# Kernel optimization log

Measured on AMD Instinct MI355X. Metric: run time of the kernel, lower is better.

The kernel has to match this reference:

```python
import jax, jax.numpy as jnp
import numpy as np

E, C, L, B = 8, 128, 1024, 32
FB = L // 2 + 1        # 513 freq bins
HD = 2 * FB            # 1026 hidden dim


def setup_inputs() -> dict:
    key = jax.random.key(0)
    ks = jax.random.split(key, 8)
    return {
        "X_time": jax.random.normal(ks[0], (B, C, L), jnp.float32),
        "bound_params": jax.random.normal(ks[1], (E - 1,), jnp.float32),
        "W1r": jax.random.normal(ks[2], (E, HD, FB), jnp.float32) * 0.1,
        "W1i": jax.random.normal(ks[3], (E, HD, FB), jnp.float32) * 0.1,
        "b1r": jnp.zeros((E, HD), jnp.float32),
        "b1i": jnp.zeros((E, HD), jnp.float32),
        "W2r": jax.random.normal(ks[4], (E, FB, HD), jnp.float32) * 0.1,
        "W2i": jax.random.normal(ks[5], (E, FB, HD), jnp.float32) * 0.1,
        "b2r": jnp.zeros((E, FB), jnp.float32),
        "b2i": jnp.zeros((E, FB), jnp.float32),
        "gate_W": jax.random.normal(ks[6], (E, FB), jnp.float32) * 0.1,
        "gate_b": jnp.zeros((E,), jnp.float32),
    }


def reference(X_time, bound_params, W1r, W1i, b1r, b1i, W2r, W2i, b2r, b2i, gate_W, gate_b):
    Bx, Cx, Lx = X_time.shape
    fb = Lx // 2 + 1
    e = W1r.shape[0]

    Xf = jnp.fft.rfft(X_time, axis=-1)                     # [B,C,FB] complex

    # learnable frequency-band binary masks
    raw = jax.nn.sigmoid(bound_params)
    bounds = jnp.sort(jnp.concatenate([jnp.zeros(1, raw.dtype), raw, jnp.ones(1, raw.dtype)]))
    idx = (bounds * (fb - 1)).astype(jnp.int32)
    starts = idx[:e]
    ends = jnp.concatenate([idx[1:e], jnp.array([fb], jnp.int32)])
    pos = jnp.arange(fb)
    masks = ((pos[None, :] >= starts[:, None]) & (pos[None, :] < ends[:, None])).astype(X_time.dtype)  # [E,FB]

    # masked spectra per expert, split into real/imag: [E,B,C,FB]
    m = masks[:, None, None, :]
    xr = Xf.real * m
    xi = Xf.imag * m

    # expert layer 1: complex linear (W [E,HD,FB]) + complex ReLU
    hr = jnp.einsum('ehf,ebcf->ebch', W1r, xr) - jnp.einsum('ehf,ebcf->ebch', W1i, xi) + b1r[:, None, None, :]
    hi = jnp.einsum('ehf,ebcf->ebch', W1r, xi) + jnp.einsum('ehf,ebcf->ebch', W1i, xr) + b1i[:, None, None, :]
    hr = jax.nn.relu(hr)
    hi = jax.nn.relu(hi)

    # expert layer 2: complex linear (W [E,FB,HD]) -> [E,B,C,FB]
    yr = jnp.einsum('efh,ebch->ebcf', W2r, hr) - jnp.einsum('efh,ebch->ebcf', W2i, hi) + b2r[:, None, None, :]
    yi = jnp.einsum('efh,ebch->ebcf', W2r, hi) + jnp.einsum('efh,ebch->ebcf', W2i, hr) + b2i[:, None, None, :]

    # gate: mean |Xf| over channels -> linear -> softmax over experts
    mag = jnp.mean(jnp.abs(Xf), axis=1)                    # [B,FB]
    gate = jax.nn.softmax(mag @ gate_W.T + gate_b, axis=-1)  # [B,E]

    comb_r = jnp.einsum('ebcf,be->bcf', yr, gate)
    comb_i = jnp.einsum('ebcf,be->bcf', yi, gate)
    return jnp.fft.irfft(jax.lax.complex(comb_r, comb_i), n=Lx, axis=-1)
```

## Files before the change

### kernel.cpp

```cpp
#include <hip/hip_runtime.h>
#include <hip/hip_bf16.h>
#include <math.h>

typedef __hip_bfloat16 bf16;
typedef __attribute__((ext_vector_type(8))) short short8;
typedef __attribute__((ext_vector_type(4))) float f32x4;

#define FB 513
#define HD 1026
#define NN 1024
#define MR 4096
#define NE 8
#define BATCH 32

#define XINT_LD 1280
#define BIAS_LD 1056
#define FINV_LD 1088
#define HP_LD   2080
#define B1_ROWS 2176
#define KCAT    16640
#define MAG_LD  520
#define FF_ROWS 1280

__device__ __forceinline__ void gload16(const void* g, void* l) {
    __builtin_amdgcn_global_load_lds((const __attribute__((address_space(1))) void*)g,
                                     (__attribute__((address_space(3))) void*)l, 16, 0, 0);
}
__device__ __forceinline__ bf16 f2b(float v) { return __float2bfloat16(v); }
__device__ __forceinline__ unsigned short f2bu(float v) {
    bf16 b = __float2bfloat16(v);
    return *reinterpret_cast<unsigned short*>(&b);
}
__device__ __forceinline__ float bu2f(unsigned short u) {
    return __uint_as_float(((unsigned)u) << 16);
}
__device__ __forceinline__ unsigned pack2(float a, float b) {
    return (unsigned)f2bu(a) | ((unsigned)f2bu(b) << 16);
}

__device__ __forceinline__ void xcd_swizzle(int* px, int* py) {
    int gx = gridDim.x;
    int orig = blockIdx.x + gx * blockIdx.y;
    int q = (gx * gridDim.y) >> 3;
    int wg = (orig & 7) * q + (orig >> 3);
    *px = wg % gx;
    *py = wg / gx;
}

__device__ __forceinline__ void compute_bounds(const float* __restrict__ bp, int* idx) {
    float b[9];
    b[0] = 0.0f; b[8] = 1.0f;
    for (int i = 0; i < 7; i++) b[i + 1] = 1.0f / (1.0f + expf(-bp[i]));
    for (int i = 1; i < 9; i++) { float v = b[i]; int j = i - 1;
        while (j >= 0 && b[j] > v) { b[j + 1] = b[j]; j--; } b[j + 1] = v; }
    for (int i = 0; i < 9; i++) idx[i] = (int)(b[i] * (float)(FB - 1));
}

#define N_FF  ((long)FF_ROWS * NN)
#define N_FI  (1024L * FINV_LD)
#define N_B1P ((long)NE * B1_ROWS * (XINT_LD / 2))
#define N_XP  ((long)MR * NN / 2)
#define N_PREP (N_FF + N_FI + N_B1P + N_XP)

__global__ void prep_bulk(const float* __restrict__ W1r, const float* __restrict__ W1i,
                          const float* __restrict__ X, const float* __restrict__ bp,
                          int* __restrict__ se,
                          bf16* __restrict__ Ffwd, bf16* __restrict__ Finv,
                          bf16* __restrict__ B1, bf16* __restrict__ Xb) {
    __shared__ int sse[16];
    if (threadIdx.x == 0) {
        int idx[9];
        compute_bounds(bp, idx);
        for (int e = 0; e < NE; e++) {
            sse[2 * e] = idx[e];
            sse[2 * e + 1] = (e < NE - 1) ? idx[e + 1] : FB;
        }
        if (blockIdx.x == 0)
            for (int k = 0; k < 16; k++) se[k] = sse[k];
    }
    __syncthreads();

    long i = (long)blockIdx.x * 256 + threadIdx.x;
    const float TWO_PI = 6.283185307179586f;
    if (i < N_FF) {
        int n = (int)(i >> 10), t = (int)(i & (NN - 1));
        float v = 0.0f;
        if (n < 2 * FB) {
            int f = n >> 1, k = (f * t) & (NN - 1);
            float s, c; sincosf(TWO_PI * (float)k / (float)NN, &s, &c);
            v = (n & 1) ? -s : c;
        }
        Ffwd[i] = f2b(v);
        return;
    }
    i -= N_FF;
    if (i < N_FI) {
        int t = (int)(i / FINV_LD), k = (int)(i % FINV_LD);
        float v = 0.0f;
        if (k < 2 * FB) {
            int f = k >> 1, kk = (f * t) & (NN - 1);
            float s, c; sincosf(TWO_PI * (float)kk / (float)NN, &s, &c);
            float cf = (f == 0 || f == FB - 1) ? 1.0f : 2.0f;
            float sc = cf * (1.0f / (float)NN);
            v = (k & 1) ? -s * sc : c * sc;
        }
        Finv[i] = f2b(v);
        return;
    }
    i -= N_FI;
    if (i < N_B1P) {
        int f = (int)(i % (XINT_LD / 2));
        long t = i / (XINT_LD / 2);
        int n = (int)(t % B1_ROWS);
        int e = (int)(t / B1_ROWS);
        float ve = 0.0f, vo = 0.0f;
        if (n < 2 * HD && f < FB && f >= sse[2 * e] && f < sse[2 * e + 1]) {
            int hi_part = (n >= HD);
            int h = hi_part ? n - HD : n;
            long wi = ((long)e * HD + h) * FB + f;
            float wr = W1r[wi], wim = W1i[wi];
            ve = hi_part ? wim : wr;
            vo = hi_part ? wr : -wim;
        }
        *(unsigned*)(B1 + ((size_t)(e * B1_ROWS + n)) * XINT_LD + 2 * f) = pack2(ve, vo);
        return;
    }
    i -= N_B1P;
    if (i < N_XP) {
        float2 v = ((const float2*)X)[i];
        *(unsigned*)(Xb + 2 * i) = pack2(v.x, v.y);
    }
}

__global__ void pack_B2t(const float* __restrict__ W2r, const float* __restrict__ W2i,
                         bf16* __restrict__ B2t) {
    __shared__ float sR[64][65], sI[64][65];
    int e = blockIdx.z;
    int f0 = blockIdx.x * 64;
    int h0 = blockIdx.y * 64;
    int tid = threadIdx.x;
#pragma unroll
    for (int rep = 0; rep < 16; rep++) {
        int idx = tid + rep * 256;
        int fl = idx >> 6, hl = idx & 63;
        int f = f0 + fl, h = h0 + hl;
        bool ok = (f < FB) && (h < HD);
        size_t wi = ((size_t)e * FB + f) * HD + h;
        sR[fl][hl] = ok ? W2r[wi] : 0.0f;
        sI[fl][hl] = ok ? W2i[wi] : 0.0f;
    }
    __syncthreads();
#pragma unroll
    for (int rep = 0; rep < 4; rep++) {
        int idx = tid + rep * 256;
        int hl = idx >> 4, ch = idx & 15;
        int h = h0 + hl;
        int c0 = 2 * f0 + ch * 8;
        if (c0 >= FINV_LD) continue;
        short8 lo, hi;
#pragma unroll
        for (int j = 0; j < 4; j++) {
            int fl = ch * 4 + j;
            float wr = sR[fl][hl], wim = sI[fl][hl];
            lo[2 * j]     = (short)f2bu(wr);
            lo[2 * j + 1] = (short)f2bu(wim);
            hi[2 * j]     = (short)f2bu(-wim);
            hi[2 * j + 1] = (short)f2bu(wr);
        }
        if (h < HD) {
            *(short8*)(B2t + ((size_t)e * HP_LD + h) * FINV_LD + c0) = lo;
            *(short8*)(B2t + ((size_t)e * HP_LD + HD + h) * FINV_LD + c0) = hi;
        } else if (HD + h < HP_LD) {
            short8 z = {};
            *(short8*)(B2t + ((size_t)e * HP_LD + HD + h) * FINV_LD + c0) = z;
        }
    }
}

__global__ void mag_kernel(const bf16* __restrict__ Xint, float* __restrict__ magp) {
    int b = blockIdx.x, g = blockIdx.y, t = threadIdx.x;
    float acc[3] = {0.0f, 0.0f, 0.0f};
    const bf16* base = Xint + ((size_t)b * 128 + g * 16) * XINT_LD;
    for (int c = 0; c < 16; c++) {
        const bf16* row = base + (size_t)c * XINT_LD;
#pragma unroll
        for (int kk = 0; kk < 3; kk++) {
            int f = t + 256 * kk;
            if (f < FB) {
                float xr = __bfloat162float(row[2 * f]);
                float xi = __bfloat162float(row[2 * f + 1]);
                acc[kk] += sqrtf(xr * xr + xi * xi);
            }
        }
    }
#pragma unroll
    for (int kk = 0; kk < 3; kk++) {
        int f = t + 256 * kk;
        if (f < FB) magp[((size_t)b * 8 + g) * MAG_LD + f] = acc[kk];
    }
}

__global__ void gate_bias_kernel(const float* __restrict__ magp, const float* __restrict__ gW,
                                 const float* __restrict__ gb, const float* __restrict__ b2r,
                                 const float* __restrict__ b2i, float* __restrict__ gate,
                                 float* __restrict__ biasCs) {
    __shared__ float sred[256];
    __shared__ float sg[8];
    int b = blockIdx.x, tid = threadIdx.x;
    int e = tid & 7, j = tid >> 3;
    float acc = 0.0f;
    for (int f = j; f < FB; f += 32) {
        float m = 0.0f;
#pragma unroll
        for (int g = 0; g < 8; g++) m += magp[((size_t)b * 8 + g) * MAG_LD + f];
        acc += m * (1.0f / 128.0f) * gW[e * FB + f];
    }
    sred[tid] = acc;
    __syncthreads();
    if (tid < 64) {
        float a = sred[tid] + sred[tid + 64] + sred[tid + 128] + sred[tid + 192];
        a += __shfl_xor(a, 8); a += __shfl_xor(a, 16); a += __shfl_xor(a, 32);
        float logit = a + gb[e];
        float mx = logit;
        mx = fmaxf(mx, __shfl_xor(mx, 1)); mx = fmaxf(mx, __shfl_xor(mx, 2)); mx = fmaxf(mx, __shfl_xor(mx, 4));
        float ex = expf(logit - mx);
        float sum = ex;
        sum += __shfl_xor(sum, 1); sum += __shfl_xor(sum, 2); sum += __shfl_xor(sum, 4);
        if (tid < 8) { float g_ = ex / sum; sg[tid] = g_; gate[b * NE + tid] = g_; }
    }
    __syncthreads();
    for (int c = tid; c < BIAS_LD; c += 256) {
        float v = 0.0f;
        if (c < 2 * FB) {
            int f = c >> 1;
            const float* bb = (c & 1) ? b2i : b2r;
#pragma unroll
            for (int ee = 0; ee < NE; ee++) v += sg[ee] * bb[ee * FB + f];
            float cf = (f == 0 || f == FB - 1) ? 1.0f : 2.0f;
            v *= cf * (1.0f / (float)NN);
        }
        biasCs[b * BIAS_LD + c] = v;
    }
}

__global__ void biasT_kernel(const float* __restrict__ biasCs, const bf16* __restrict__ Ffwd,
                             float* __restrict__ biasT) {
    int t = blockIdx.x * 256 + threadIdx.x;
    int b = blockIdx.y;
    float s = 0.0f;
    for (int c = 0; c < 2 * FB; c++)
        s += biasCs[b * BIAS_LD + c] * __bfloat162float(Ffwd[(size_t)c * NN + t]);
    biasT[b * NN + t] = s;
}

__global__ void reduce_out4(const bf16* __restrict__ planes, const float* __restrict__ biasT,
                            float* __restrict__ out) {
    long idx = (long)blockIdx.x * 256 + threadIdx.x;
    if (idx >= (long)MR * NN / 8) return;
    size_t base = (size_t)idx * 8;
    long r = base >> 10;
    int t = (int)(base & (NN - 1));
    float s[8] = {};
#pragma unroll
    for (int z = 0; z < 4; z++) {
        short8 v = *(const short8*)(planes + (size_t)z * MR * NN + base);
#pragma unroll
        for (int j = 0; j < 8; j++) s[j] += bu2f((unsigned short)v[j]);
    }
    const float* bT = biasT + (r >> 7) * NN + t;
    float4 o0 = {s[0] + bT[0], s[1] + bT[1], s[2] + bT[2], s[3] + bT[3]};
    float4 o1 = {s[4] + bT[4], s[5] + bT[5], s[6] + bT[6], s[7] + bT[7]};
    *(float4*)(out + base) = o0;
    *(float4*)(out + base + 4) = o1;
}

template <int EPI>
__global__ void gemm_mfma(const bf16* __restrict__ A, int lda,
                          const bf16* __restrict__ B, int ldb, size_t zBstride,
                          void* __restrict__ Cv, int ldc, size_t zCoff,
                          int N, int K, int kPerZ,
                          const int* __restrict__ se2,
                          const float* __restrict__ biasR, const float* __restrict__ biasI,
                          int zBias, const float* __restrict__ gate8) {
    __shared__ bf16 As[128 * 32];
    __shared__ bf16 Bs[128 * 32];
    int tid = threadIdx.x;
    int zz = blockIdx.z;
    int bx, by;
    xcd_swizzle(&bx, &by);
    int row0 = by * 128, col0 = bx * 128;
    const bf16* Bz = B + (size_t)zz * zBstride;

    int kS, kE;
    if (EPI == 1) { int s = se2[2 * zz], e = se2[2 * zz + 1]; kS = (2 * s) & ~31; kE = (2 * e + 31) & ~31; }
    else          { kS = zz * kPerZ; kE = min(K, kS + kPerZ); }

    f32x4 acc[4][4] = {};

    int lane = tid & 63, wid = tid >> 6;
    int wrB = (wid >> 1) << 6, wcB = (wid & 1) << 6;
    int lr = lane & 15, lk = (lane >> 4) << 3;

    int r_a = tid >> 2, c_a = (tid & 3) << 3;
    int r_b = (tid + 256) >> 2, c_b = ((tid + 256) & 3) << 3;

    for (int kt = kS; kt < kE; kt += 32) {
        gload16(A + (size_t)(row0 + r_a) * lda + kt + c_a, &As[(size_t)tid * 8]);
        gload16(A + (size_t)(row0 + r_b) * lda + kt + c_b, &As[((size_t)tid + 256) * 8]);
        gload16(Bz + (size_t)(col0 + r_a) * ldb + kt + c_a, &Bs[(size_t)tid * 8]);
        gload16(Bz + (size_t)(col0 + r_b) * ldb + kt + c_b, &Bs[((size_t)tid + 256) * 8]);
        __syncthreads();
        short8 av[4], bv[4];
#pragma unroll
        for (int m = 0; m < 4; m++)
            av[m] = *(const short8*)&As[(wrB + m * 16 + lr) * 32 + lk];
#pragma unroll
        for (int n = 0; n < 4; n++)
            bv[n] = *(const short8*)&Bs[(wcB + n * 16 + lr) * 32 + lk];
#pragma unroll
        for (int m = 0; m < 4; m++)
#pragma unroll
            for (int n = 0; n < 4; n++)
                acc[m][n] = __builtin_amdgcn_mfma_f32_16x16x32_bf16(av[m], bv[n], acc[m][n], 0, 0, 0);
        __syncthreads();
    }

    int r0 = row0 + wrB + ((lane >> 4) << 2);
    int c0i = col0 + wcB + (lane & 15);
    float g = (EPI == 1) ? gate8[(row0 >> 7) * NE + zz] : 0.0f;

#pragma unroll
    for (int m = 0; m < 4; m++)
#pragma unroll
        for (int n = 0; n < 4; n++) {
            int c = c0i + n * 16;
            if (c >= N) continue;
#pragma unroll
            for (int j = 0; j < 4; j++) {
                int r = r0 + m * 16 + j;
                float v = acc[m][n][j];
                if (EPI == 1) {
                    v += (c < HD) ? biasR[zz * zBias + c] : biasI[zz * zBias + c - HD];
                    v = fmaxf(v, 0.0f) * g;
                    ((bf16*)Cv + (size_t)zz * zCoff)[(size_t)r * ldc + c] = f2b(v);
                } else {
                    ((float*)Cv + (size_t)zz * zCoff)[(size_t)r * ldc + c] = v;
                }
            }
        }
}

__device__ __forceinline__ void stage_half(const bf16* gbase, int ld, int kt,
                                           bf16* ldsBase, int tid) {
#pragma unroll
    for (int j = 0; j < 2; j++) {
        int r = j * 64 + (tid >> 3);
        int sc = ((tid & 7) ^ ((tid >> 3) & 7)) * 8;
        gload16(gbase + (size_t)r * ld + kt + sc, ldsBase + j * 4096 + tid * 8);
    }
}

#define MF(a, b, c) __builtin_amdgcn_mfma_f32_16x16x32_bf16(a, b, c, 0, 0, 0)
#define RD(off) (*(const short8*)(bc + (off)))
#define LOADA(dst, FM)                                                        \
    dst[0] = RD(aBase + (FM) * 1024 + cb0);                                   \
    dst[1] = RD(aBase + (FM) * 1024 + cb1);                                   \
    dst[2] = RD(aBase + (FM + 1) * 1024 + cb0);                               \
    dst[3] = RD(aBase + (FM + 1) * 1024 + cb1);
#define CLUST(FM, av)                                                         \
    __builtin_amdgcn_s_setprio(1);                                            \
    acc[FM][0] = MF(av[0], b0[0], acc[FM][0]);                                \
    acc[FM][0] = MF(av[1], b1[0], acc[FM][0]);                                \
    acc[FM][1] = MF(av[0], b0[1], acc[FM][1]);                                \
    acc[FM][1] = MF(av[1], b1[1], acc[FM][1]);                                \
    acc[FM][2] = MF(av[0], b0[2], acc[FM][2]);                                \
    acc[FM][2] = MF(av[1], b1[2], acc[FM][2]);                                \
    acc[FM][3] = MF(av[0], b0[3], acc[FM][3]);                                \
    acc[FM][3] = MF(av[1], b1[3], acc[FM][3]);                                \
    acc[FM + 1][0] = MF(av[2], b0[0], acc[FM + 1][0]);                        \
    acc[FM + 1][0] = MF(av[3], b1[0], acc[FM + 1][0]);                        \
    acc[FM + 1][1] = MF(av[2], b0[1], acc[FM + 1][1]);                        \
    acc[FM + 1][1] = MF(av[3], b1[1], acc[FM + 1][1]);                        \
    acc[FM + 1][2] = MF(av[2], b0[2], acc[FM + 1][2]);                        \
    acc[FM + 1][2] = MF(av[3], b1[2], acc[FM + 1][2]);                        \
    acc[FM + 1][3] = MF(av[2], b0[3], acc[FM + 1][3]);                        \
    acc[FM + 1][3] = MF(av[3], b1[3], acc[FM + 1][3]);                        \
    __builtin_amdgcn_s_setprio(0);
#define PBAR { __builtin_amdgcn_sched_barrier(0); __builtin_amdgcn_s_barrier(); }

template <int SWZ>
__global__ __launch_bounds__(512, 2) void gemm8p(
        const bf16* __restrict__ A, int lda, const bf16* __restrict__ B, int ldb,
        bf16* __restrict__ C, int ldc, size_t zCoff,
        int tilesPerZ, int totTiles, int gx) {
    __shared__ bf16 sm[65536];
    int tid = threadIdx.x;
    int id = blockIdx.x;
    int bx, by, z;
    if (SWZ == 1) {
        int by_z = (id & 7) * 8 + (id >> 5);
        bx = (id >> 3) & 3;
        z = by_z >> 4;
        by = by_z & 15;
    } else {
        bx = id % gx; by = id / gx; z = 0;
    }
    int row0 = by * 256, col0 = bx * 256;
    int t0 = z * tilesPerZ;
    int nt = min(tilesPerZ, totTiles - t0);
    int kS = t0 * 64;

    const bf16* Ab = A + (size_t)row0 * lda;
    const bf16* Bb = B + (size_t)col0 * ldb;

    stage_half(Ab, lda, kS, sm, tid);
    stage_half(Ab + (size_t)128 * lda, lda, kS, sm + 8192, tid);
    stage_half(Bb, ldb, kS, sm + 16384, tid);
    stage_half(Bb + (size_t)128 * ldb, ldb, kS, sm + 24576, tid);

    f32x4 acc[8][4] = {};

    int l = tid & 63, w = tid >> 6;
    int wm = w >> 2, wn = w & 3;
    int lr = l & 15, lk4 = l >> 4;
    int swz = lr & 7;
    int cb0 = ((lk4) ^ swz) * 8;
    int cb1 = ((4 + lk4) ^ swz) * 8;
    int aBase = wm * 8192 + lr * 64;
    int bBase = 16384 + (wn >> 1) * 8192 + (wn & 1) * 4096 + lr * 64;

    for (int t = 0; t < nt; ++t) {
        const int cur = t & 1;
        const bf16* bc = sm + cur * 32768;
        bf16* bufN = sm + (cur ^ 1) * 32768;
        int ktn = kS + (t + 1) * 64;
        bool more = (t + 1) < nt;
        if (more) {
            stage_half(Ab, lda, ktn, bufN, tid);
            stage_half(Ab + (size_t)128 * lda, lda, ktn, bufN + 8192, tid);
            asm volatile("s_waitcnt vmcnt(4)" ::: "memory");
        } else {
            asm volatile("s_waitcnt vmcnt(0)" ::: "memory");
        }
        __builtin_amdgcn_s_barrier();
        __builtin_amdgcn_sched_barrier(0);
        short8 b0[4], b1[4], a0[4], a1[4], a2[4], a3[4];
#pragma unroll
        for (int n = 0; n < 4; n++) {
            b0[n] = RD(bBase + n * 1024 + cb0);
            b1[n] = RD(bBase + n * 1024 + cb1);
        }
        LOADA(a0, 0)
        LOADA(a1, 2)
        __builtin_amdgcn_sched_barrier(0);
        CLUST(0, a0)
        if (more) {
            stage_half(Bb, ldb, ktn, bufN + 16384, tid);
            stage_half(Bb + (size_t)128 * ldb, ldb, ktn, bufN + 24576, tid);
        }
        LOADA(a2, 4)
        PBAR
        CLUST(2, a1)
        LOADA(a3, 6)
        PBAR
        CLUST(4, a2)
        PBAR
        CLUST(6, a3)
        PBAR
    }

    bf16* Cp = C + (size_t)z * zCoff;
    int rb = row0 + wm * 128 + lk4 * 4;
    int cbase = col0 + wn * 64 + lr;
#pragma unroll
    for (int fm = 0; fm < 8; fm++)
#pragma unroll
        for (int n = 0; n < 4; n++)
#pragma unroll
            for (int j = 0; j < 4; j++)
                Cp[(size_t)(rb + fm * 16 + j) * ldc + cbase + n * 16] = f2b(acc[fm][n][j]);
}

extern "C" void kernel_launch(void* const* d_in, const int* in_sizes, int n_in,
                              void* d_out, int out_size, void* d_ws, size_t ws_size,
                              hipStream_t stream) {
    const float* X   = (const float*)d_in[0];
    const float* bp  = (const float*)d_in[1];
    const float* W1r = (const float*)d_in[2];
    const float* W1i = (const float*)d_in[3];
    const float* b1r = (const float*)d_in[4];
    const float* b1i = (const float*)d_in[5];
    const float* W2r = (const float*)d_in[6];
    const float* W2i = (const float*)d_in[7];
    const float* b2r = (const float*)d_in[8];
    const float* b2i = (const float*)d_in[9];
    const float* gW  = (const float*)d_in[10];
    const float* gb  = (const float*)d_in[11];
    float* out = (float*)d_out;

    const size_t SZH = (size_t)MR * HP_LD * 2;

    char* p = (char*)d_ws;
    auto alloc = [&](size_t bytes) -> char* {
        char* r = p; p += (bytes + 255) & ~255ULL; return r;
    };
    int*   se     = (int*)alloc(64 * 4);
    float* magp   = (float*)alloc((size_t)BATCH * 8 * MAG_LD * 4);
    float* gate   = (float*)alloc((size_t)BATCH * NE * 4);
    float* biasCs = (float*)alloc((size_t)BATCH * BIAS_LD * 4);
    float* biasT  = (float*)alloc((size_t)BATCH * NN * 4);
    bf16*  Ffwd   = (bf16*)alloc((size_t)FF_ROWS * NN * 2);
    bf16*  Finv   = (bf16*)alloc((size_t)NN * FINV_LD * 2);
    bf16*  B1     = (bf16*)alloc((size_t)NE * B1_ROWS * XINT_LD * 2);
    bf16*  B2t    = (bf16*)alloc((size_t)KCAT * FINV_LD * 2);
    bf16*  Xint   = (bf16*)alloc((size_t)MR * XINT_LD * 2);
    bf16*  planesB = (bf16*)alloc(4 * (size_t)MR * NN * 2);
    bf16*  Hp     = (bf16*)alloc(8 * SZH);
    bf16*  B2inv  = (bf16*)B1;
    bf16*  Xb     = (bf16*)((char*)Hp + 8 * SZH - (size_t)MR * NN * 2);

    prep_bulk<<<(unsigned)((N_PREP + 255) / 256), 256, 0, stream>>>(
        W1r, W1i, X, bp, se, Ffwd, Finv, B1, Xb);
    pack_B2t<<<dim3(9, 17, 8), 256, 0, stream>>>(W2r, W2i, B2t);

    gemm8p<0><<<80, 512, 0, stream>>>(
        Xb, NN, Ffwd, NN, Xint, XINT_LD, 0, 16, 16, 5);

    mag_kernel<<<dim3(BATCH, 8), 256, 0, stream>>>(Xint, magp);
    gate_bias_kernel<<<BATCH, 256, 0, stream>>>(magp, gW, gb, b2r, b2i, gate, biasCs);
    biasT_kernel<<<dim3(4, BATCH), 256, 0, stream>>>(biasCs, Ffwd, biasT);

    gemm_mfma<1><<<dim3(17, 32, 8), 256, 0, stream>>>(
        Xint, XINT_LD, B1, XINT_LD, (size_t)B1_ROWS * XINT_LD,
        Hp, KCAT, HP_LD, 2 * HD, 0, 0,
        se, b1r, b1i, HD, gate);

    gemm8p<0><<<260, 512, 0, stream>>>(
        Finv, FINV_LD, B2t, FINV_LD, B2inv, KCAT, 0, 17, 17, 65);

    gemm8p<1><<<256, 512, 0, stream>>>(
        Hp, KCAT, B2inv, KCAT, planesB, NN, (size_t)MR * NN, 65, 260, 4);

    reduce_out4<<<(unsigned)(((size_t)MR * NN / 8 + 255) / 256), 256, 0, stream>>>(
        planesB, biasT, out);
}
```

Baseline: 423.7 us.

## Merge DFT GEMM and B2inv precompute into one launch; hoist bounds kernel

The small forward-DFT GEMM (80 blocks) and the independent Finv×B2t precompute GEMM (260 blocks) now run as a single 340-block launch. Each block picks its problem from its block index, so the small GEMM no longer leaves most CUs idle on its own. The frequency-bound sigmoid and sort now run once in a tiny separate kernel, instead of serially on thread 0 of every prep_bulk block behind a barrier. Workspace aliasing is reorganised to match: B2inv gets its own buffer because it is now produced before B1 is consumed, and planesB reuses B1's storage. The cost is an extra tiny launch and more workspace memory.

```diff
diff --git a/kernel.cpp b/kernel.cpp
--- a/kernel.cpp
+++ b/kernel.cpp
@@ -47,13 +47,20 @@
     *py = wg / gx;
 }
 
-__device__ __forceinline__ void compute_bounds(const float* __restrict__ bp, int* idx) {
-    float b[9];
-    b[0] = 0.0f; b[8] = 1.0f;
-    for (int i = 0; i < 7; i++) b[i + 1] = 1.0f / (1.0f + expf(-bp[i]));
-    for (int i = 1; i < 9; i++) { float v = b[i]; int j = i - 1;
-        while (j >= 0 && b[j] > v) { b[j + 1] = b[j]; j--; } b[j + 1] = v; }
-    for (int i = 0; i < 9; i++) idx[i] = (int)(b[i] * (float)(FB - 1));
+__global__ void prep_kernel(const float* __restrict__ bp, int* __restrict__ se) {
+    if (threadIdx.x == 0 && blockIdx.x == 0) {
+        float b[9];
+        b[0] = 0.0f; b[8] = 1.0f;
+        for (int i = 0; i < 7; i++) b[i + 1] = 1.0f / (1.0f + expf(-bp[i]));
+        for (int i = 1; i < 9; i++) { float v = b[i]; int j = i - 1;
+            while (j >= 0 && b[j] > v) { b[j + 1] = b[j]; j--; } b[j + 1] = v; }
+        int idx[9];
+        for (int i = 0; i < 9; i++) idx[i] = (int)(b[i] * (float)(FB - 1));
+        for (int e = 0; e < NE; e++) {
+            se[2 * e] = idx[e];
+            se[2 * e + 1] = (e < NE - 1) ? idx[e + 1] : FB;
+        }
+    }
 }
 
 #define N_FF  ((long)FF_ROWS * NN)
@@ -63,23 +70,9 @@
 #define N_PREP (N_FF + N_FI + N_B1P + N_XP)
 
 __global__ void prep_bulk(const float* __restrict__ W1r, const float* __restrict__ W1i,
-                          const float* __restrict__ X, const float* __restrict__ bp,
-                          int* __restrict__ se,
+                          const float* __restrict__ X, const int* __restrict__ se,
                           bf16* __restrict__ Ffwd, bf16* __restrict__ Finv,
                           bf16* __restrict__ B1, bf16* __restrict__ Xb) {
-    __shared__ int sse[16];
-    if (threadIdx.x == 0) {
-        int idx[9];
-        compute_bounds(bp, idx);
-        for (int e = 0; e < NE; e++) {
-            sse[2 * e] = idx[e];
-            sse[2 * e + 1] = (e < NE - 1) ? idx[e + 1] : FB;
-        }
-        if (blockIdx.x == 0)
-            for (int k = 0; k < 16; k++) se[k] = sse[k];
-    }
-    __syncthreads();
-
     long i = (long)blockIdx.x * 256 + threadIdx.x;
     const float TWO_PI = 6.283185307179586f;
     if (i < N_FF) {
@@ -114,7 +107,7 @@
         int n = (int)(t % B1_ROWS);
         int e = (int)(t / B1_ROWS);
         float ve = 0.0f, vo = 0.0f;
-        if (n < 2 * HD && f < FB && f >= sse[2 * e] && f < sse[2 * e + 1]) {
+        if (n < 2 * HD && f < FB && f >= se[2 * e] && f < se[2 * e + 1]) {
             int hi_part = (n >= HD);
             int h = hi_part ? n - HD : n;
             long wi = ((long)e * HD + h) * FB + f;
@@ -388,28 +381,12 @@
     __builtin_amdgcn_s_setprio(0);
 #define PBAR { __builtin_amdgcn_sched_barrier(0); __builtin_amdgcn_s_barrier(); }
 
-template <int SWZ>
-__global__ __launch_bounds__(512, 2) void gemm8p(
-        const bf16* __restrict__ A, int lda, const bf16* __restrict__ B, int ldb,
-        bf16* __restrict__ C, int ldc, size_t zCoff,
-        int tilesPerZ, int totTiles, int gx) {
-    __shared__ bf16 sm[65536];
+__device__ __forceinline__ void gemm8p_body(
+        bf16* sm, const bf16* __restrict__ A, int lda,
+        const bf16* __restrict__ B, int ldb,
+        bf16* __restrict__ C, int ldc,
+        int row0, int col0, int kS, int nt) {
     int tid = threadIdx.x;
-    int id = blockIdx.x;
-    int bx, by, z;
-    if (SWZ == 1) {
-        int by_z = (id & 7) * 8 + (id >> 5);
-        bx = (id >> 3) & 3;
-        z = by_z >> 4;
-        by = by_z & 15;
-    } else {
-        bx = id % gx; by = id / gx; z = 0;
-    }
-    int row0 = by * 256, col0 = bx * 256;
-    int t0 = z * tilesPerZ;
-    int nt = min(tilesPerZ, totTiles - t0);
-    int kS = t0 * 64;
-
     const bf16* Ab = A + (size_t)row0 * lda;
     const bf16* Bb = B + (size_t)col0 * ldb;
 
@@ -469,7 +446,6 @@
         PBAR
     }
 
-    bf16* Cp = C + (size_t)z * zCoff;
     int rb = row0 + wm * 128 + lk4 * 4;
     int cbase = col0 + wn * 64 + lr;
 #pragma unroll
@@ -478,7 +454,37 @@
         for (int n = 0; n < 4; n++)
 #pragma unroll
             for (int j = 0; j < 4; j++)
-                Cp[(size_t)(rb + fm * 16 + j) * ldc + cbase + n * 16] = f2b(acc[fm][n][j]);
+                C[(size_t)(rb + fm * 16 + j) * ldc + cbase + n * 16] = f2b(acc[fm][n][j]);
+}
+
+__global__ __launch_bounds__(512, 2) void gemm8p_combo(
+        const bf16* A0, int lda0, const bf16* B0, int ldb0, bf16* C0, int ldc0,
+        int gx0, int nt0, int nb0,
+        const bf16* A1, int lda1, const bf16* B1w, int ldb1, bf16* C1, int ldc1,
+        int gx1, int nt1) {
+    __shared__ bf16 sm[65536];
+    int id = blockIdx.x;
+    bool p0 = id < nb0;
+    const bf16* A = p0 ? A0 : A1; int lda = p0 ? lda0 : lda1;
+    const bf16* B = p0 ? B0 : B1w; int ldb = p0 ? ldb0 : ldb1;
+    bf16* C = p0 ? C0 : C1; int ldc = p0 ? ldc0 : ldc1;
+    int gx = p0 ? gx0 : gx1, nt = p0 ? nt0 : nt1;
+    int id2 = p0 ? id : id - nb0;
+    int bx = id2 % gx, by = id2 / gx;
+    gemm8p_body(sm, A, lda, B, ldb, C, ldc, by * 256, bx * 256, 0, nt);
+}
+
+__global__ __launch_bounds__(512, 2) void gemm8p_l2(
+        const bf16* __restrict__ A, int lda, const bf16* __restrict__ B, int ldb,
+        bf16* __restrict__ C, int ldc, size_t zCoff, int tilesPerZ) {
+    __shared__ bf16 sm[65536];
+    int id = blockIdx.x;
+    int by_z = (id & 7) * 8 + (id >> 5);
+    int bx = (id >> 3) & 3;
+    int z = by_z >> 4;
+    int by = by_z & 15;
+    gemm8p_body(sm, A, lda, B, ldb, C + (size_t)z * zCoff, ldc,
+                by * 256, bx * 256, z * tilesPerZ * 64, tilesPerZ);
 }
 
 extern "C" void kernel_launch(void* const* d_in, const int* in_sizes, int n_in,
@@ -511,20 +517,23 @@
     float* biasT  = (float*)alloc((size_t)BATCH * NN * 4);
     bf16*  Ffwd   = (bf16*)alloc((size_t)FF_ROWS * NN * 2);
     bf16*  Finv   = (bf16*)alloc((size_t)NN * FINV_LD * 2);
-    bf16*  B1     = (bf16*)alloc((size_t)NE * B1_ROWS * XINT_LD * 2);
+    char*  b1slot = alloc((size_t)NE * B1_ROWS * XINT_LD * 2);
+    bf16*  B1     = (bf16*)b1slot;
+    bf16*  planesB = (bf16*)b1slot;
     bf16*  B2t    = (bf16*)alloc((size_t)KCAT * FINV_LD * 2);
     bf16*  Xint   = (bf16*)alloc((size_t)MR * XINT_LD * 2);
-    bf16*  planesB = (bf16*)alloc(4 * (size_t)MR * NN * 2);
+    bf16*  B2inv  = (bf16*)alloc((size_t)NN * KCAT * 2);
     bf16*  Hp     = (bf16*)alloc(8 * SZH);
-    bf16*  B2inv  = (bf16*)B1;
     bf16*  Xb     = (bf16*)((char*)Hp + 8 * SZH - (size_t)MR * NN * 2);
 
+    prep_kernel<<<1, 64, 0, stream>>>(bp, se);
     prep_bulk<<<(unsigned)((N_PREP + 255) / 256), 256, 0, stream>>>(
-        W1r, W1i, X, bp, se, Ffwd, Finv, B1, Xb);
+        W1r, W1i, X, se, Ffwd, Finv, B1, Xb);
     pack_B2t<<<dim3(9, 17, 8), 256, 0, stream>>>(W2r, W2i, B2t);
 
-    gemm8p<0><<<80, 512, 0, stream>>>(
-        Xb, NN, Ffwd, NN, Xint, XINT_LD, 0, 16, 16, 5);
+    gemm8p_combo<<<340, 512, 0, stream>>>(
+        Finv, FINV_LD, B2t, FINV_LD, B2inv, KCAT, 65, 17, 260,
+        Xb, NN, Ffwd, NN, Xint, XINT_LD, 5, 16);
 
     mag_kernel<<<dim3(BATCH, 8), 256, 0, stream>>>(Xint, magp);
     gate_bias_kernel<<<BATCH, 256, 0, stream>>>(magp, gW, gb, b2r, b2i, gate, biasCs);
@@ -535,11 +544,8 @@
         Hp, KCAT, HP_LD, 2 * HD, 0, 0,
         se, b1r, b1i, HD, gate);
 
-    gemm8p<0><<<260, 512, 0, stream>>>(
-        Finv, FINV_LD, B2t, FINV_LD, B2inv, KCAT, 0, 17, 17, 65);
-
-    gemm8p<1><<<256, 512, 0, stream>>>(
-        Hp, KCAT, B2inv, KCAT, planesB, NN, (size_t)MR * NN, 65, 260, 4);
+    gemm8p_l2<<<256, 512, 0, stream>>>(
+        Hp, KCAT, B2inv, KCAT, planesB, NN, (size_t)MR * NN, 65);
 
     reduce_out4<<<(unsigned)(((size_t)MR * NN / 8 + 255) / 256), 256, 0, stream>>>(
         planesB, biasT, out);
```

Result: faster. 379.8 us (-10.4%).
